# Kernel tuning notes

Hardware: AMD Instinct MI355X
Metric: run time of the kernel (lower is better)

Reference implementation:

```python
import jax, jax.numpy as jnp
import numpy as np

DIM = 768
NUM_HEADS = 12
DIM_HEAD = 64
INNER = NUM_HEADS * DIM_HEAD  # 768
SCALE = DIM_HEAD ** -0.5


def setup_inputs() -> dict:
    key = jax.random.key(0)
    k1, k2, k3 = jax.random.split(key, 3)
    B, N = 8, 1024
    x = jax.random.normal(k1, (B, N, DIM), dtype=jnp.float32)
    # Linear(dim, 3*inner_dim, bias=False): weight shape (out, in) torch-style
    w_qkv = jax.random.normal(k2, (3 * INNER, DIM), dtype=jnp.float32) * (DIM ** -0.5)
    # proj: Linear(inner_dim, dim, bias=False)
    w_proj = jax.random.normal(k3, (DIM, INNER), dtype=jnp.float32) * (INNER ** -0.5)
    return {"x": x, "w_qkv": w_qkv, "w_proj": w_proj}


def reference(x, w_qkv, w_proj):
    B, N, C = x.shape
    H, dh = NUM_HEADS, DIM_HEAD
    # qkv projection: (B,N,C) @ (C, 3*inner) -> (B,N,3*inner)
    qkv = jnp.einsum('bnc,oc->bno', x, w_qkv)
    qkv = qkv.reshape(B, N, 3, H, dh).transpose(2, 0, 3, 1, 4)  # (3,B,H,N,dh)
    q, k, v = qkv[0], qkv[1], qkv[2]
    # attention scores (B,H,N,N)
    attn_scores = jnp.einsum('bhnd,bhmd->bhnm', q, k) * SCALE
    attn_probs = jax.nn.softmax(attn_scores, axis=-1)
    # attention output (B,H,N,dh) -> (B,N,inner)
    attn_out = jnp.einsum('bhnm,bhmd->bhnd', attn_probs, v)
    attn_out = attn_out.transpose(0, 2, 1, 3).reshape(B, N, H * dh)
    out = jnp.einsum('bni,oi->bno', attn_out, w_proj)
    return out
```

## Files before the change

### kernel.cpp

```cpp
#include <hip/hip_runtime.h>
#include <stdint.h>

typedef unsigned short u16;
typedef __attribute__((ext_vector_type(8))) short short8;
typedef __attribute__((ext_vector_type(4))) short short4v;
typedef __attribute__((ext_vector_type(4))) float f32x4;

#define LOG2E 1.44269504088896340736f

#define Bb 8
#define NSEQ 1024
#define DIMC 768
#define NH 12
#define DH 64
#define INNER 768
#define MTOT (Bb*NSEQ)
#define QKVN (3*INNER)
#define HEADS_TOT (Bb*NH)
#define QKV_PART ((size_t)Bb*NH*NSEQ*DH)

static __device__ inline u16 f2bf(float f) {
    uint32_t u = __builtin_bit_cast(uint32_t, f);
    uint32_t r = (u + 0x7fffu + ((u >> 16) & 1u)) >> 16;
    return (u16)r;
}

static __device__ __forceinline__ uint32_t pkbf(float f0, float f1) {
    uint32_t u0 = __builtin_bit_cast(uint32_t, f0) + 0x8000u;
    uint32_t u1 = __builtin_bit_cast(uint32_t, f1) + 0x8000u;
    return __builtin_amdgcn_perm(u1, u0, 0x07060302u);
}

#if __has_builtin(__builtin_amdgcn_mfma_f32_16x16x16bf16_1k)
static __device__ __forceinline__ f32x4 mfma16(short4v a, short4v b, f32x4 c) {
    return __builtin_amdgcn_mfma_f32_16x16x16bf16_1k(a, b, c, 0, 0, 0);
}
#else
static __device__ __forceinline__ f32x4 mfma16(short4v a, short4v b, f32x4 c) {
    asm volatile("v_mfma_f32_16x16x16_bf16 %0, %1, %2, %0\n\ts_nop 7\n\ts_nop 7"
                 : "+v"(c) : "v"(a), "v"(b));
    return c;
}
#endif

typedef __attribute__((address_space(1))) const void gas_void;
typedef __attribute__((address_space(3))) void las_void;
static __device__ __forceinline__ void async16(u16* lds, const u16* g) {
    __builtin_amdgcn_global_load_lds((gas_void*)(uintptr_t)g,
                                     (las_void*)(uintptr_t)lds, 16, 0, 0);
}

template <int N>
static __device__ __forceinline__ void wait_vm() {
    __builtin_amdgcn_s_waitcnt(0x0f70 | N);
}

#define NX8  786432
#define NWQ8 221184
#define NWP8 73728
#define NCVT (NX8 + NWQ8 + NWP8)
__global__ __launch_bounds__(256) void cvt_all(const float* __restrict__ x,
                                               const float* __restrict__ wq,
                                               const float* __restrict__ wp,
                                               u16* __restrict__ xb,
                                               u16* __restrict__ wqb,
                                               u16* __restrict__ wpb) {
    int i = blockIdx.x * 256 + threadIdx.x;
    const float* s; u16* d; int j;
    if (i < NX8) { s = x; d = xb; j = i; }
    else if (i < NX8 + NWQ8) { s = wq; d = wqb; j = i - NX8; }
    else { s = wp; d = wpb; j = i - NX8 - NWQ8; }
    const float4* s4 = (const float4*)s;
    float4 a = s4[2 * j], b = s4[2 * j + 1];
    float v[8] = {a.x, a.y, a.z, a.w, b.x, b.y, b.z, b.w};
    u16 o[8];
#pragma unroll
    for (int t = 0; t < 8; t++) o[t] = f2bf(v[t]);
    ((uint4*)d)[j] = *(const uint4*)o;
}

#define BK 32
__global__ __launch_bounds__(512, 4) void gemm_qkv(const u16* __restrict__ A,
                                                   const u16* __restrict__ Bm,
                                                   u16* __restrict__ qkv) {
    __shared__ u16 As[3][128 * BK];
    __shared__ u16 Bs[3][256 * BK];
    const int tid = threadIdx.x;
    const int w = tid >> 6, lane = tid & 63, quad = lane >> 4, l16 = lane & 15;
    const int wr = w >> 2, wc = w & 3;
    const int bid = blockIdx.x + 9 * blockIdx.y;
    const int xcd = bid & 7, j9 = bid >> 3;
    const int m0 = (8 * xcd + j9 / 9) * 128;
    const int n0 = (j9 % 9) * 256;
    const int K = DIMC;

    const int rl = lane >> 2, cc = lane & 3;
    const int ra = w * 16 + rl;
    const u16* agp = A + (size_t)(m0 + ra) * K + ((cc - ((ra >> 1) & 3)) & 3) * 8;
    const int aslot = (w * 16) * BK;
    const u16* bgp[2]; int bslot[2];
#pragma unroll
    for (int j = 0; j < 2; j++) {
        int rb = w * 32 + j * 16 + rl;
        bgp[j] = Bm + (size_t)(n0 + rb) * K + ((cc - ((rb >> 1) & 3)) & 3) * 8;
        bslot[j] = (w * 32 + j * 16) * BK;
    }

    const int swz = ((quad + ((l16 >> 1) & 3)) & 3) * 8;
    int aoff[4], boff[4];
#pragma unroll
    for (int t = 0; t < 4; t++) {
        aoff[t] = (wr * 64 + t * 16 + l16) * BK + swz;
        boff[t] = (wc * 64 + t * 16 + l16) * BK + swz;
    }

#pragma unroll
    for (int tt = 0; tt < 2; tt++) {
        int kt = tt * BK;
        async16(&As[tt][aslot], agp + kt);
        async16(&Bs[tt][bslot[0]], bgp[0] + kt);
        async16(&Bs[tt][bslot[1]], bgp[1] + kt);
    }

    f32x4 acc[4][4] = {};
    const int NIT = K / BK;
    int cur = 0;
    for (int it = 0; it < NIT; ++it) {
        if (it < NIT - 1) wait_vm<3>();
        else              wait_vm<0>();
        __builtin_amdgcn_s_barrier();
        if (it < NIT - 2) {
            int pre = cur + 2; if (pre >= 3) pre -= 3;
            int ktn = (it + 2) * BK;
            async16(&As[pre][aslot], agp + ktn);
            async16(&Bs[pre][bslot[0]], bgp[0] + ktn);
            async16(&Bs[pre][bslot[1]], bgp[1] + ktn);
        }
        short8 af[4], bf[4];
#pragma unroll
        for (int t = 0; t < 4; t++) af[t] = *(const short8*)(&As[cur][aoff[t]]);
#pragma unroll
        for (int t = 0; t < 4; t++) bf[t] = *(const short8*)(&Bs[cur][boff[t]]);
#pragma unroll
        for (int mt = 0; mt < 4; mt++)
#pragma unroll
            for (int nt = 0; nt < 4; nt++)
                acc[mt][nt] = __builtin_amdgcn_mfma_f32_16x16x32_bf16(af[mt], bf[nt],
                                                                      acc[mt][nt], 0, 0, 0);
        cur = (cur == 2) ? 0 : cur + 1;
    }

#pragma unroll
    for (int nt = 0; nt < 4; nt++) {
        int o = n0 + wc * 64 + nt * 16 + l16;
        int which = o / 768;
        int rem = o - which * 768;
        int h = rem >> 6, d = rem & 63;
        if (which == 2) {
            u16* vt = qkv + 2 * QKV_PART;
#pragma unroll
            for (int mt = 0; mt < 4; mt++) {
                int m = m0 + wr * 64 + mt * 16 + quad * 4;
                int bb = m >> 10, ns = m & 1023;
                alignas(8) u16 pk[4];
#pragma unroll
                for (int r = 0; r < 4; r++) pk[r] = f2bf(acc[mt][nt][r]);
                *(uint2*)(vt + ((size_t)(bb * NH + h) * DH + d) * NSEQ + ns) =
                    *(const uint2*)pk;
            }
        } else {
            float sc = (which == 0) ? (0.125f * LOG2E) : 1.0f;
#pragma unroll
            for (int mt = 0; mt < 4; mt++)
#pragma unroll
                for (int r = 0; r < 4; r++) {
                    int m = m0 + wr * 64 + mt * 16 + quad * 4 + r;
                    int bb = m >> 10, ns = m & 1023;
                    size_t idx = (size_t)which * QKV_PART +
                                 (((size_t)(bb * NH + h) * NSEQ + ns) << 6) + d;
                    qkv[idx] = f2bf(acc[mt][nt][r] * sc);
                }
        }
    }
}

#define PBM 64
#define PBN 128
__global__ __launch_bounds__(256) void gemm_proj(const u16* __restrict__ A,
                                                 const u16* __restrict__ Bm,
                                                 float* __restrict__ Co) {
    __shared__ u16 As[3][PBM * BK];
    __shared__ u16 Bs[3][PBN * BK];
    const int tid = threadIdx.x;
    const int w = tid >> 6, lane = tid & 63, quad = lane >> 4, l16 = lane & 15;
    const int wr = w >> 1, wc = w & 1;
    const int m0 = blockIdx.y * PBM;
    const int n0 = blockIdx.x * PBN;
    const int K = INNER, N = DIMC;

    const int rl = lane >> 2, cc = lane & 3;
    const int ra = w * 16 + rl;
    const u16* agp = A + (size_t)(m0 + ra) * K + ((cc - ((ra >> 1) & 3)) & 3) * 8;
    const int aslot = (w * 16) * BK;
    const u16* bgp[2]; int bslot[2];
#pragma unroll
    for (int j = 0; j < 2; j++) {
        int rb = j * 64 + w * 16 + rl;
        bgp[j] = Bm + (size_t)(n0 + rb) * K + ((cc - ((rb >> 1) & 3)) & 3) * 8;
        bslot[j] = (j * 64 + w * 16) * BK;
    }
    const int swz = ((quad + ((l16 >> 1) & 3)) & 3) * 8;
    int aoff[2], boff[4];
#pragma unroll
    for (int t = 0; t < 2; t++) aoff[t] = (wr * 32 + t * 16 + l16) * BK + swz;
#pragma unroll
    for (int t = 0; t < 4; t++) boff[t] = (wc * 64 + t * 16 + l16) * BK + swz;

#pragma unroll
    for (int tt = 0; tt < 2; tt++) {
        int kt = tt * BK;
        async16(&As[tt][aslot], agp + kt);
        async16(&Bs[tt][bslot[0]], bgp[0] + kt);
        async16(&Bs[tt][bslot[1]], bgp[1] + kt);
    }

    f32x4 acc[2][4] = {};
    const int NIT = K / BK;
    int cur = 0;
    for (int it = 0; it < NIT; ++it) {
        if (it < NIT - 1) wait_vm<3>(); else wait_vm<0>();
        __builtin_amdgcn_s_barrier();
        if (it < NIT - 2) {
            int pre = cur + 2; if (pre >= 3) pre -= 3;
            int ktn = (it + 2) * BK;
            async16(&As[pre][aslot], agp + ktn);
            async16(&Bs[pre][bslot[0]], bgp[0] + ktn);
            async16(&Bs[pre][bslot[1]], bgp[1] + ktn);
        }
        short8 af[2], bf[4];
#pragma unroll
        for (int t = 0; t < 2; t++) af[t] = *(const short8*)(&As[cur][aoff[t]]);
#pragma unroll
        for (int t = 0; t < 4; t++) bf[t] = *(const short8*)(&Bs[cur][boff[t]]);
#pragma unroll
        for (int mt = 0; mt < 2; mt++)
#pragma unroll
            for (int nt = 0; nt < 4; nt++)
                acc[mt][nt] = __builtin_amdgcn_mfma_f32_16x16x32_bf16(af[mt], bf[nt],
                                                                      acc[mt][nt], 0, 0, 0);
        cur = (cur == 2) ? 0 : cur + 1;
    }
#pragma unroll
    for (int mt = 0; mt < 2; mt++)
#pragma unroll
        for (int nt = 0; nt < 4; nt++) {
            int o = n0 + wc * 64 + nt * 16 + l16;
#pragma unroll
            for (int r = 0; r < 4; r++) {
                int m = m0 + wr * 32 + mt * 16 + quad * 4 + r;
                Co[(size_t)m * N + o] = acc[mt][nt][r];
            }
        }
}

__global__ __launch_bounds__(256) void attn_kernel(const u16* __restrict__ qkv,
                                                   u16* __restrict__ attn) {
    __shared__ u16 Ks[3][64 * 64];
    __shared__ u16 Vs[3][64 * 64];

    const int tid = threadIdx.x;
    const int w = tid >> 6, lane = tid & 63, quad = lane >> 4, l16 = lane & 15;
    const int bh = blockIdx.x, qt = blockIdx.y;
    const size_t headoff = (size_t)bh * NSEQ * DH;
    const u16* Qp = qkv + headoff;
    const u16* Kp = qkv + QKV_PART + headoff;
    const u16* Vtp = qkv + 2 * QKV_PART + headoff;
    const int q0 = qt * 128 + w * 32;

    const int rl8 = lane >> 3, cc8 = lane & 7;
    const u16* kg[2]; const u16* vg[2]; int ksl[2];
#pragma unroll
    for (int j = 0; j < 2; j++) {
        int r = w * 16 + j * 8 + rl8;
        int c = ((cc8 - r) & 7) * 8;
        kg[j] = Kp + (size_t)r * DH + c;
        vg[j] = Vtp + (size_t)r * NSEQ + c;
        ksl[j] = (w * 16 + j * 8) * 64;
    }

    const int sw0 = ((quad + l16) & 7) * 8;
    const int sw1 = ((quad + 4 + l16) & 7) * 8;

    short8 qf[2][2];
#pragma unroll
    for (int mf = 0; mf < 2; mf++) {
        qf[mf][0] = *(const short8*)(Qp + (size_t)(q0 + mf * 16 + l16) * DH + quad * 8);
        qf[mf][1] = *(const short8*)(Qp + (size_t)(q0 + mf * 16 + l16) * DH + 32 + quad * 8);
    }

#pragma unroll
    for (int tt = 0; tt < 3; tt++) {
        int kt = tt * 64;
#pragma unroll
        for (int j = 0; j < 2; j++) {
            async16(&Ks[tt][ksl[j]], kg[j] + (size_t)kt * DH);
            async16(&Vs[tt][ksl[j]], vg[j] + kt);
        }
    }
    asm volatile("" :: "v"(qf[0][0]), "v"(qf[0][1]), "v"(qf[1][0]), "v"(qf[1][1]));

    f32x4 oacc[2][4] = {};
    float lsum[2] = {0.f, 0.f};

    const int NIT = NSEQ / 64;
    int cur = 0;
    for (int it = 0; it < NIT; ++it) {
        if (it == 0)          wait_vm<8>();
        else if (it < NIT - 1) wait_vm<4>();
        else                   wait_vm<0>();
        __builtin_amdgcn_s_barrier();
        if (it >= 1 && it < NIT - 2) {
            int pre = cur + 2; if (pre >= 3) pre -= 3;
            int ktn = (it + 2) * 64;
#pragma unroll
            for (int j = 0; j < 2; j++) {
                async16(&Ks[pre][ksl[j]], kg[j] + (size_t)ktn * DH);
                async16(&Vs[pre][ksl[j]], vg[j] + ktn);
            }
        }

        short8 kf[4][2];
#pragma unroll
        for (int nt = 0; nt < 4; nt++) {
            const u16* kr = &Ks[cur][(nt * 16 + l16) * 64];
            kf[nt][0] = *(const short8*)(kr + sw0);
            kf[nt][1] = *(const short8*)(kr + sw1);
        }
        short4v vf[4][4];
#pragma unroll
        for (int nt2 = 0; nt2 < 4; nt2++) {
            int row = nt2 * 16 + l16;
#pragma unroll
            for (int c = 0; c < 4; c++) {
                int off = row * 64 + (((c * 2 + (quad >> 1) + row) & 7) << 3) + (quad & 1) * 4;
                vf[nt2][c] = *(const short4v*)(&Vs[cur][off]);
            }
        }

#pragma unroll
        for (int mf = 0; mf < 2; mf++) {
            f32x4 st[4];
#pragma unroll
            for (int nt = 0; nt < 4; nt++) {
                f32x4 z = {};
                z = __builtin_amdgcn_mfma_f32_16x16x32_bf16(kf[nt][0], qf[mf][0], z, 0, 0, 0);
                z = __builtin_amdgcn_mfma_f32_16x16x32_bf16(kf[nt][1], qf[mf][1], z, 0, 0, 0);
                st[nt] = z;
            }
            short4v pf[4];
#pragma unroll
            for (int c = 0; c < 4; c++) {
                float p0 = __builtin_amdgcn_exp2f(st[c][0]);
                float p1 = __builtin_amdgcn_exp2f(st[c][1]);
                float p2 = __builtin_amdgcn_exp2f(st[c][2]);
                float p3 = __builtin_amdgcn_exp2f(st[c][3]);
                lsum[mf] += (p0 + p1) + (p2 + p3);
                uint2 u = {pkbf(p0, p1), pkbf(p2, p3)};
                pf[c] = __builtin_bit_cast(short4v, u);
            }
#pragma unroll
            for (int nt2 = 0; nt2 < 4; nt2++)
#pragma unroll
                for (int c = 0; c < 4; c++)
                    oacc[mf][nt2] = mfma16(vf[nt2][c], pf[c], oacc[mf][nt2]);
        }
        cur = (cur == 2) ? 0 : cur + 1;
    }

#pragma unroll
    for (int mf = 0; mf < 2; mf++) {
        float v = lsum[mf];
        v += __shfl_xor(v, 16);
        v += __shfl_xor(v, 32);
        lsum[mf] = 1.0f / v;
    }

    const int b = bh / NH, h = bh - (bh / NH) * NH;
#pragma unroll
    for (int mf = 0; mf < 2; mf++) {
        int q = q0 + mf * 16 + l16;
        float inv = lsum[mf];
#pragma unroll
        for (int nt2 = 0; nt2 < 4; nt2++) {
            uint2 u = {pkbf(oacc[mf][nt2][0] * inv, oacc[mf][nt2][1] * inv),
                       pkbf(oacc[mf][nt2][2] * inv, oacc[mf][nt2][3] * inv)};
            int d = nt2 * 16 + quad * 4;
            *(uint2*)(attn + ((size_t)(b * NSEQ + q)) * INNER + h * DH + d) = u;
        }
    }
}

extern "C" void kernel_launch(void* const* d_in, const int* in_sizes, int n_in,
                              void* d_out, int out_size, void* d_ws, size_t ws_size,
                              hipStream_t stream) {
    const float* x = (const float*)d_in[0];
    const float* w_qkv = (const float*)d_in[1];
    const float* w_proj = (const float*)d_in[2];
    float* out = (float*)d_out;

    u16* xb = (u16*)d_ws;
    u16* wqkvb = xb + 6291456;
    u16* wprojb = wqkvb + 1769472;
    u16* qkvb = wprojb + 589824;
    u16* attnb = qkvb + 18874368;

    cvt_all<<<NCVT / 256, 256, 0, stream>>>(x, w_qkv, w_proj, xb, wqkvb, wprojb);

    dim3 g1(QKVN / 256, MTOT / 128);
    gemm_qkv<<<g1, 512, 0, stream>>>(xb, wqkvb, qkvb);

    dim3 g2(HEADS_TOT, NSEQ / 128);
    attn_kernel<<<g2, 256, 0, stream>>>(qkvb, attnb);

    dim3 g3(INNER / PBN, MTOT / PBM);
    gemm_proj<<<g3, 256, 0, stream>>>(attnb, wprojb, out);
}
```

Baseline: 185.9 us.

## Replace triple-buffered async GEMM pipelines with single-buffer sync loops and smaller QKV tiles

Both GEMMs drop their three-stage async-to-LDS ring buffers for a single LDS buffer that is loaded, synchronized, computed and synchronized again each K step. The QKV GEMM moves from 512-thread 128x256 tiles to 256-thread 128x128 tiles with an adjusted XCD-aware block mapping, and the projection GEMM gains an occupancy hint. The attention kernel changes its wait counts, adds a scheduling barrier after the block barrier, and moves a register-pinning asm before the prefetch. Less LDS per block may allow more resident blocks, but global load latency is no longer overlapped with MFMA work inside a block.

```diff
diff --git a/kernel.cpp b/kernel.cpp
--- a/kernel.cpp
+++ b/kernel.cpp
@@ -52,7 +52,13 @@
 
 template <int N>
 static __device__ __forceinline__ void wait_vm() {
-    __builtin_amdgcn_s_waitcnt(0x0f70 | N);
+    constexpr int simm = 0x0f70 | (N & 15) | ((N >> 4) << 14);
+    __builtin_amdgcn_s_waitcnt(simm);
+}
+
+static __device__ __forceinline__ void block_barrier() {
+    __builtin_amdgcn_s_barrier();
+    __builtin_amdgcn_sched_barrier(0);
 }
 
 #define NX8  786432
@@ -80,30 +86,29 @@
 }
 
 #define BK 32
-__global__ __launch_bounds__(512, 4) void gemm_qkv(const u16* __restrict__ A,
+__global__ __launch_bounds__(256, 4) void gemm_qkv(const u16* __restrict__ A,
                                                    const u16* __restrict__ Bm,
                                                    u16* __restrict__ qkv) {
-    __shared__ u16 As[3][128 * BK];
-    __shared__ u16 Bs[3][256 * BK];
+    __shared__ u16 As[128 * BK];
+    __shared__ u16 Bs[128 * BK];
     const int tid = threadIdx.x;
     const int w = tid >> 6, lane = tid & 63, quad = lane >> 4, l16 = lane & 15;
-    const int wr = w >> 2, wc = w & 3;
-    const int bid = blockIdx.x + 9 * blockIdx.y;
-    const int xcd = bid & 7, j9 = bid >> 3;
-    const int m0 = (8 * xcd + j9 / 9) * 128;
-    const int n0 = (j9 % 9) * 256;
+    const int wr = w >> 1, wc = w & 1;
+    const int bid = blockIdx.x + 18 * blockIdx.y;
+    const int xcd = bid & 7, j18 = bid >> 3;
+    const int m0 = (8 * xcd + j18 / 18) * 128;
+    const int n0 = (j18 % 18) * 128;
     const int K = DIMC;
 
     const int rl = lane >> 2, cc = lane & 3;
-    const int ra = w * 16 + rl;
-    const u16* agp = A + (size_t)(m0 + ra) * K + ((cc - ((ra >> 1) & 3)) & 3) * 8;
-    const int aslot = (w * 16) * BK;
-    const u16* bgp[2]; int bslot[2];
+    const u16* agp[2]; const u16* bgp[2]; int sl[2];
 #pragma unroll
     for (int j = 0; j < 2; j++) {
-        int rb = w * 32 + j * 16 + rl;
-        bgp[j] = Bm + (size_t)(n0 + rb) * K + ((cc - ((rb >> 1) & 3)) & 3) * 8;
-        bslot[j] = (w * 32 + j * 16) * BK;
+        int r = j * 64 + w * 16 + rl;
+        int c = ((cc - ((r >> 1) & 3)) & 3) * 8;
+        agp[j] = A + (size_t)(m0 + r) * K + c;
+        bgp[j] = Bm + (size_t)(n0 + r) * K + c;
+        sl[j] = (j * 64 + w * 16) * BK;
     }
 
     const int swz = ((quad + ((l16 >> 1) & 3)) & 3) * 8;
@@ -114,40 +119,28 @@
         boff[t] = (wc * 64 + t * 16 + l16) * BK + swz;
     }
 
-#pragma unroll
-    for (int tt = 0; tt < 2; tt++) {
-        int kt = tt * BK;
-        async16(&As[tt][aslot], agp + kt);
-        async16(&Bs[tt][bslot[0]], bgp[0] + kt);
-        async16(&Bs[tt][bslot[1]], bgp[1] + kt);
-    }
-
     f32x4 acc[4][4] = {};
     const int NIT = K / BK;
-    int cur = 0;
     for (int it = 0; it < NIT; ++it) {
-        if (it < NIT - 1) wait_vm<3>();
-        else              wait_vm<0>();
-        __builtin_amdgcn_s_barrier();
-        if (it < NIT - 2) {
-            int pre = cur + 2; if (pre >= 3) pre -= 3;
-            int ktn = (it + 2) * BK;
-            async16(&As[pre][aslot], agp + ktn);
-            async16(&Bs[pre][bslot[0]], bgp[0] + ktn);
-            async16(&Bs[pre][bslot[1]], bgp[1] + ktn);
-        }
+        int kt = it * BK;
+#pragma unroll
+        for (int j = 0; j < 2; j++) {
+            async16(&As[sl[j]], agp[j] + kt);
+            async16(&Bs[sl[j]], bgp[j] + kt);
+        }
+        __syncthreads();
         short8 af[4], bf[4];
 #pragma unroll
-        for (int t = 0; t < 4; t++) af[t] = *(const short8*)(&As[cur][aoff[t]]);
-#pragma unroll
-        for (int t = 0; t < 4; t++) bf[t] = *(const short8*)(&Bs[cur][boff[t]]);
+        for (int t = 0; t < 4; t++) af[t] = *(const short8*)(&As[aoff[t]]);
+#pragma unroll
+        for (int t = 0; t < 4; t++) bf[t] = *(const short8*)(&Bs[boff[t]]);
 #pragma unroll
         for (int mt = 0; mt < 4; mt++)
 #pragma unroll
             for (int nt = 0; nt < 4; nt++)
                 acc[mt][nt] = __builtin_amdgcn_mfma_f32_16x16x32_bf16(af[mt], bf[nt],
                                                                       acc[mt][nt], 0, 0, 0);
-        cur = (cur == 2) ? 0 : cur + 1;
+        __syncthreads();
     }
 
 #pragma unroll
@@ -186,11 +179,11 @@
 
 #define PBM 64
 #define PBN 128
-__global__ __launch_bounds__(256) void gemm_proj(const u16* __restrict__ A,
-                                                 const u16* __restrict__ Bm,
-                                                 float* __restrict__ Co) {
-    __shared__ u16 As[3][PBM * BK];
-    __shared__ u16 Bs[3][PBN * BK];
+__global__ __launch_bounds__(256, 4) void gemm_proj(const u16* __restrict__ A,
+                                                    const u16* __restrict__ Bm,
+                                                    float* __restrict__ Co) {
+    __shared__ u16 As[PBM * BK];
+    __shared__ u16 Bs[PBN * BK];
     const int tid = threadIdx.x;
     const int w = tid >> 6, lane = tid & 63, quad = lane >> 4, l16 = lane & 15;
     const int wr = w >> 1, wc = w & 1;
@@ -216,39 +209,26 @@
 #pragma unroll
     for (int t = 0; t < 4; t++) boff[t] = (wc * 64 + t * 16 + l16) * BK + swz;
 
-#pragma unroll
-    for (int tt = 0; tt < 2; tt++) {
-        int kt = tt * BK;
-        async16(&As[tt][aslot], agp + kt);
-        async16(&Bs[tt][bslot[0]], bgp[0] + kt);
-        async16(&Bs[tt][bslot[1]], bgp[1] + kt);
-    }
-
     f32x4 acc[2][4] = {};
     const int NIT = K / BK;
-    int cur = 0;
     for (int it = 0; it < NIT; ++it) {
-        if (it < NIT - 1) wait_vm<3>(); else wait_vm<0>();
-        __builtin_amdgcn_s_barrier();
-        if (it < NIT - 2) {
-            int pre = cur + 2; if (pre >= 3) pre -= 3;
-            int ktn = (it + 2) * BK;
-            async16(&As[pre][aslot], agp + ktn);
-            async16(&Bs[pre][bslot[0]], bgp[0] + ktn);
-            async16(&Bs[pre][bslot[1]], bgp[1] + ktn);
-        }
+        int kt = it * BK;
+        async16(&As[aslot], agp + kt);
+        async16(&Bs[bslot[0]], bgp[0] + kt);
+        async16(&Bs[bslot[1]], bgp[1] + kt);
+        __syncthreads();
         short8 af[2], bf[4];
 #pragma unroll
-        for (int t = 0; t < 2; t++) af[t] = *(const short8*)(&As[cur][aoff[t]]);
-#pragma unroll
-        for (int t = 0; t < 4; t++) bf[t] = *(const short8*)(&Bs[cur][boff[t]]);
+        for (int t = 0; t < 2; t++) af[t] = *(const short8*)(&As[aoff[t]]);
+#pragma unroll
+        for (int t = 0; t < 4; t++) bf[t] = *(const short8*)(&Bs[boff[t]]);
 #pragma unroll
         for (int mt = 0; mt < 2; mt++)
 #pragma unroll
             for (int nt = 0; nt < 4; nt++)
                 acc[mt][nt] = __builtin_amdgcn_mfma_f32_16x16x32_bf16(af[mt], bf[nt],
                                                                       acc[mt][nt], 0, 0, 0);
-        cur = (cur == 2) ? 0 : cur + 1;
+        __syncthreads();
     }
 #pragma unroll
     for (int mt = 0; mt < 2; mt++)
@@ -297,6 +277,7 @@
         qf[mf][0] = *(const short8*)(Qp + (size_t)(q0 + mf * 16 + l16) * DH + quad * 8);
         qf[mf][1] = *(const short8*)(Qp + (size_t)(q0 + mf * 16 + l16) * DH + 32 + quad * 8);
     }
+    asm volatile("" :: "v"(qf[0][0]), "v"(qf[0][1]), "v"(qf[1][0]), "v"(qf[1][1]));
 
 #pragma unroll
     for (int tt = 0; tt < 3; tt++) {
@@ -307,7 +288,6 @@
             async16(&Vs[tt][ksl[j]], vg[j] + kt);
         }
     }
-    asm volatile("" :: "v"(qf[0][0]), "v"(qf[0][1]), "v"(qf[1][0]), "v"(qf[1][1]));
 
     f32x4 oacc[2][4] = {};
     float lsum[2] = {0.f, 0.f};
@@ -315,10 +295,9 @@
     const int NIT = NSEQ / 64;
     int cur = 0;
     for (int it = 0; it < NIT; ++it) {
-        if (it == 0)          wait_vm<8>();
-        else if (it < NIT - 1) wait_vm<4>();
-        else                   wait_vm<0>();
-        __builtin_amdgcn_s_barrier();
+        if (it < NIT - 1) wait_vm<4>();
+        else              wait_vm<0>();
+        block_barrier();
         if (it >= 1 && it < NIT - 2) {
             int pre = cur + 2; if (pre >= 3) pre -= 3;
             int ktn = (it + 2) * 64;
@@ -416,8 +395,8 @@
 
     cvt_all<<<NCVT / 256, 256, 0, stream>>>(x, w_qkv, w_proj, xb, wqkvb, wprojb);
 
-    dim3 g1(QKVN / 256, MTOT / 128);
-    gemm_qkv<<<g1, 512, 0, stream>>>(xb, wqkvb, qkvb);
+    dim3 g1(QKVN / 128, MTOT / 128);
+    gemm_qkv<<<g1, 256, 0, stream>>>(xb, wqkvb, qkvb);
 
     dim3 g2(HEADS_TOT, NSEQ / 128);
     attn_kernel<<<g2, 256, 0, stream>>>(qkvb, attnb);
```

After: 187.2 us. About the same (+0.7%).

## Add MFMA setprio hints, sched barriers, and single-buffer the projection GEMM

Applied to the files above, without the earlier changes.

Wraps MFMA sections of the QKV GEMM and attention kernels in s_setprio so waves issuing matrix ops get priority, and adds a sched_barrier after each block barrier to stop the compiler reordering across it. The projection GEMM drops its triple-buffered async pipeline for a single buffer with __syncthreads, which cuts LDS use so launch_bounds(256,4) can raise occupancy, at the cost of no load/compute overlap inside a block. The waitcnt encoding now also writes the high vmcnt bits, and the attention kernel's first-iteration wait drops from vmcnt 8 to 4. The Q-fragment asm pin also moves ahead of the prologue K/V loads.

```diff
diff --git a/kernel.cpp b/kernel.cpp
--- a/kernel.cpp
+++ b/kernel.cpp
@@ -52,7 +52,13 @@
 
 template <int N>
 static __device__ __forceinline__ void wait_vm() {
-    __builtin_amdgcn_s_waitcnt(0x0f70 | N);
+    constexpr int simm = 0x0f70 | (N & 15) | ((N >> 4) << 14);
+    __builtin_amdgcn_s_waitcnt(simm);
+}
+
+static __device__ __forceinline__ void block_barrier() {
+    __builtin_amdgcn_s_barrier();
+    __builtin_amdgcn_sched_barrier(0);
 }
 
 #define NX8  786432
@@ -128,7 +134,7 @@
     for (int it = 0; it < NIT; ++it) {
         if (it < NIT - 1) wait_vm<3>();
         else              wait_vm<0>();
-        __builtin_amdgcn_s_barrier();
+        block_barrier();
         if (it < NIT - 2) {
             int pre = cur + 2; if (pre >= 3) pre -= 3;
             int ktn = (it + 2) * BK;
@@ -141,12 +147,14 @@
         for (int t = 0; t < 4; t++) af[t] = *(const short8*)(&As[cur][aoff[t]]);
 #pragma unroll
         for (int t = 0; t < 4; t++) bf[t] = *(const short8*)(&Bs[cur][boff[t]]);
+        __builtin_amdgcn_s_setprio(1);
 #pragma unroll
         for (int mt = 0; mt < 4; mt++)
 #pragma unroll
             for (int nt = 0; nt < 4; nt++)
                 acc[mt][nt] = __builtin_amdgcn_mfma_f32_16x16x32_bf16(af[mt], bf[nt],
                                                                       acc[mt][nt], 0, 0, 0);
+        __builtin_amdgcn_s_setprio(0);
         cur = (cur == 2) ? 0 : cur + 1;
     }
 
@@ -186,11 +194,11 @@
 
 #define PBM 64
 #define PBN 128
-__global__ __launch_bounds__(256) void gemm_proj(const u16* __restrict__ A,
-                                                 const u16* __restrict__ Bm,
-                                                 float* __restrict__ Co) {
-    __shared__ u16 As[3][PBM * BK];
-    __shared__ u16 Bs[3][PBN * BK];
+__global__ __launch_bounds__(256, 4) void gemm_proj(const u16* __restrict__ A,
+                                                    const u16* __restrict__ Bm,
+                                                    float* __restrict__ Co) {
+    __shared__ u16 As[PBM * BK];
+    __shared__ u16 Bs[PBN * BK];
     const int tid = threadIdx.x;
     const int w = tid >> 6, lane = tid & 63, quad = lane >> 4, l16 = lane & 15;
     const int wr = w >> 1, wc = w & 1;
@@ -216,39 +224,28 @@
 #pragma unroll
     for (int t = 0; t < 4; t++) boff[t] = (wc * 64 + t * 16 + l16) * BK + swz;
 
-#pragma unroll
-    for (int tt = 0; tt < 2; tt++) {
-        int kt = tt * BK;
-        async16(&As[tt][aslot], agp + kt);
-        async16(&Bs[tt][bslot[0]], bgp[0] + kt);
-        async16(&Bs[tt][bslot[1]], bgp[1] + kt);
-    }
-
     f32x4 acc[2][4] = {};
     const int NIT = K / BK;
-    int cur = 0;
     for (int it = 0; it < NIT; ++it) {
-        if (it < NIT - 1) wait_vm<3>(); else wait_vm<0>();
-        __builtin_amdgcn_s_barrier();
-        if (it < NIT - 2) {
-            int pre = cur + 2; if (pre >= 3) pre -= 3;
-            int ktn = (it + 2) * BK;
-            async16(&As[pre][aslot], agp + ktn);
-            async16(&Bs[pre][bslot[0]], bgp[0] + ktn);
-            async16(&Bs[pre][bslot[1]], bgp[1] + ktn);
-        }
+        int kt = it * BK;
+        async16(&As[aslot], agp + kt);
+        async16(&Bs[bslot[0]], bgp[0] + kt);
+        async16(&Bs[bslot[1]], bgp[1] + kt);
+        __syncthreads();
         short8 af[2], bf[4];
 #pragma unroll
-        for (int t = 0; t < 2; t++) af[t] = *(const short8*)(&As[cur][aoff[t]]);
-#pragma unroll
-        for (int t = 0; t < 4; t++) bf[t] = *(const short8*)(&Bs[cur][boff[t]]);
+        for (int t = 0; t < 2; t++) af[t] = *(const short8*)(&As[aoff[t]]);
+#pragma unroll
+        for (int t = 0; t < 4; t++) bf[t] = *(const short8*)(&Bs[boff[t]]);
+        __builtin_amdgcn_s_setprio(1);
 #pragma unroll
         for (int mt = 0; mt < 2; mt++)
 #pragma unroll
             for (int nt = 0; nt < 4; nt++)
                 acc[mt][nt] = __builtin_amdgcn_mfma_f32_16x16x32_bf16(af[mt], bf[nt],
                                                                       acc[mt][nt], 0, 0, 0);
-        cur = (cur == 2) ? 0 : cur + 1;
+        __builtin_amdgcn_s_setprio(0);
+        __syncthreads();
     }
 #pragma unroll
     for (int mt = 0; mt < 2; mt++)
@@ -297,6 +294,7 @@
         qf[mf][0] = *(const short8*)(Qp + (size_t)(q0 + mf * 16 + l16) * DH + quad * 8);
         qf[mf][1] = *(const short8*)(Qp + (size_t)(q0 + mf * 16 + l16) * DH + 32 + quad * 8);
     }
+    asm volatile("" :: "v"(qf[0][0]), "v"(qf[0][1]), "v"(qf[1][0]), "v"(qf[1][1]));
 
 #pragma unroll
     for (int tt = 0; tt < 3; tt++) {
@@ -307,7 +305,6 @@
             async16(&Vs[tt][ksl[j]], vg[j] + kt);
         }
     }
-    asm volatile("" :: "v"(qf[0][0]), "v"(qf[0][1]), "v"(qf[1][0]), "v"(qf[1][1]));
 
     f32x4 oacc[2][4] = {};
     float lsum[2] = {0.f, 0.f};
@@ -315,10 +312,9 @@
     const int NIT = NSEQ / 64;
     int cur = 0;
     for (int it = 0; it < NIT; ++it) {
-        if (it == 0)          wait_vm<8>();
-        else if (it < NIT - 1) wait_vm<4>();
-        else                   wait_vm<0>();
-        __builtin_amdgcn_s_barrier();
+        if (it < NIT - 1) wait_vm<4>();
+        else              wait_vm<0>();
+        block_barrier();
         if (it >= 1 && it < NIT - 2) {
             int pre = cur + 2; if (pre >= 3) pre -= 3;
             int ktn = (it + 2) * 64;
@@ -350,6 +346,7 @@
 #pragma unroll
         for (int mf = 0; mf < 2; mf++) {
             f32x4 st[4];
+            __builtin_amdgcn_s_setprio(1);
 #pragma unroll
             for (int nt = 0; nt < 4; nt++) {
                 f32x4 z = {};
@@ -357,6 +354,7 @@
                 z = __builtin_amdgcn_mfma_f32_16x16x32_bf16(kf[nt][1], qf[mf][1], z, 0, 0, 0);
                 st[nt] = z;
             }
+            __builtin_amdgcn_s_setprio(0);
             short4v pf[4];
 #pragma unroll
             for (int c = 0; c < 4; c++) {
@@ -368,11 +366,13 @@
                 uint2 u = {pkbf(p0, p1), pkbf(p2, p3)};
                 pf[c] = __builtin_bit_cast(short4v, u);
             }
+            __builtin_amdgcn_s_setprio(1);
 #pragma unroll
             for (int nt2 = 0; nt2 < 4; nt2++)
 #pragma unroll
                 for (int c = 0; c < 4; c++)
                     oacc[mf][nt2] = mfma16(vf[nt2][c], pf[c], oacc[mf][nt2]);
+            __builtin_amdgcn_s_setprio(0);
         }
         cur = (cur == 2) ? 0 : cur + 1;
     }
```

After: 192.1 us. 3.3% more time.
